# Optimization experiments

Measured on AMD Instinct MI355X. Metric: run time of the kernel, lower is better.

The kernel has to match this reference:

```python
import jax, jax.numpy as jnp
import numpy as np

BS, N, H, W, C3D, K = 2, 4096, 64, 192, 64, 3


def _leaky(x):
    return jnp.where(x >= 0, x, 0.1 * x)


def setup_inputs() -> dict:
    key = jax.random.key(0)
    ks = jax.random.split(key, 10)
    # uv: pixel coordinates (x in [0,W), y in [0,H)), channel-first [bs,2,N]
    uv = jax.random.uniform(ks[0], (BS, 2, N), dtype=jnp.float32)
    uv = uv * jnp.array([W, H], dtype=jnp.float32)[None, :, None]
    feat_2d = jax.random.normal(ks[1], (BS, 64, H, W), dtype=jnp.float32)
    feat_3d = jax.random.normal(ks[2], (BS, C3D, N), dtype=jnp.float32)
    w1 = jax.random.normal(ks[3], (16, 3), dtype=jnp.float32) * 0.3
    b1 = jax.random.normal(ks[4], (16,), dtype=jnp.float32) * 0.1
    w2 = jax.random.normal(ks[5], (C3D, 16), dtype=jnp.float32) * 0.2
    b2 = jax.random.normal(ks[6], (C3D,), dtype=jnp.float32) * 0.1
    w_out = jax.random.normal(ks[7], (C3D, C3D), dtype=jnp.float32) * 0.1
    b_out = jax.random.normal(ks[8], (C3D,), dtype=jnp.float32) * 0.1
    return {"uv": uv, "feat_2d": feat_2d, "feat_3d": feat_3d,
            "w1": w1, "b1": b1, "w2": w2, "b2": b2,
            "w_out": w_out, "b_out": b_out}


def reference(uv, feat_2d, feat_3d, w1, b1, w2, b2, w_out, b_out):
    bs, _, image_h, image_w = feat_2d.shape
    c3d = feat_3d.shape[1]
    hw = image_h * image_w

    # mesh grid, channel order (x, y), flattened row-major over (h, w): [bs,2,HW]
    ys, xs = jnp.meshgrid(jnp.arange(image_h, dtype=jnp.float32),
                          jnp.arange(image_w, dtype=jnp.float32), indexing='ij')
    grid = jnp.stack([xs.ravel(), ys.ravel()], axis=0)  # [2, HW]
    grid = jnp.broadcast_to(grid[None], (bs, 2, hw))

    # k-NN of uv points for each grid query: squared distances [bs, HW, N]
    d2 = (jnp.sum(grid * grid, axis=1)[:, :, None]
          + jnp.sum(uv * uv, axis=1)[:, None, :]
          - 2.0 * jnp.einsum('bcq,bcn->bqn', grid, uv))
    _, knn_idx = jax.lax.top_k(-d2, K)  # [bs, HW, K]

    # gather uv and feat_3d by neighbor indices: [bs, 2+C, HW, K]
    data = jnp.concatenate([uv, feat_3d], axis=1)
    knn = jax.vmap(lambda d, i: d[:, i])(data, knn_idx)
    knn_uv, knn_feat3d = knn[:, :2], knn[:, 2:]

    knn_offset = knn_uv - grid[..., None]                      # [bs,2,HW,K]
    offset_norm = jnp.linalg.norm(knn_offset, axis=1, keepdims=True)
    score_in = jnp.concatenate([knn_offset, offset_norm], 1)   # [bs,3,HW,K]

    # score net: 1x1 conv (3->16, leaky_relu 0.1) -> 1x1 conv (16->C, sigmoid)
    h1 = _leaky(jnp.einsum('bcqk,oc->boqk', score_in, w1) + b1[None, :, None, None])
    score = jax.nn.sigmoid(jnp.einsum('bcqk,oc->boqk', h1, w2) + b2[None, :, None, None])

    final = jnp.sum(score * knn_feat3d, axis=-1)               # [bs,C,HW]
    final = final.reshape(bs, c3d, image_h, image_w)

    # out conv: 1x1 conv (C->C) + leaky_relu 0.1
    out = _leaky(jnp.einsum('bchw,oc->bohw', final, w_out) + b_out[None, :, None, None])
    return out
```

## Files before the change

### kernel.cpp

```cpp
#include <hip/hip_runtime.h>
#include <math.h>

#define NBS 2
#define NPTS 4096
#define HH 64
#define WW 192
#define HW (HH*WW)
#define NC 64
#define GX 48
#define GY 16
#define NCELL (GX*GY)
#define CSB 1024

#define FBIG 3.0e38f
#define IBIG 0x7FFFFFFF

__global__ __launch_bounds__(256) void k0_prep(
    const float* __restrict__ uv, const float* __restrict__ f3d,
    float* __restrict__ f3dT, float4* __restrict__ binned,
    int* __restrict__ cellStart) {
#pragma clang fp contract(off)
  int bid = blockIdx.x;
  int t = threadIdx.x;
  if (bid < 2) {
    int b = bid;
    __shared__ int hist[NCELL];
    __shared__ int cum[NCELL];
    __shared__ int cur[NCELL];
    for (int c = t; c < NCELL; c += 256) hist[c] = 0;
    __syncthreads();
    const float* u0p = uv + (size_t)b * 2 * NPTS;
    const float* u1p = u0p + NPTS;
    for (int n = t; n < NPTS; n += 256) {
      float u0 = u0p[n], u1 = u1p[n];
      int cxp = min((int)(u0 * 0.25f), GX - 1);
      int cyp = min((int)(u1 * 0.25f), GY - 1);
      atomicAdd(&hist[cyp * GX + cxp], 1);
    }
    __syncthreads();
    if (t < 64) {
      int carry = 0;
#pragma unroll
      for (int ck = 0; ck < NCELL / 64; ++ck) {
        int v = hist[ck * 64 + t];
#pragma unroll
        for (int off = 1; off < 64; off <<= 1) {
          int u = __shfl_up(v, off);
          if (t >= off) v += u;
        }
        cum[ck * 64 + t] = v + carry;
        carry += __shfl(v, 63);
      }
    }
    __syncthreads();
    if (t == 0) cellStart[b * CSB] = 0;
    for (int c = t; c < NCELL; c += 256) {
      cellStart[b * CSB + c + 1] = cum[c];
      cur[c] = cum[c] - hist[c];
    }
    __syncthreads();
    for (int n = t; n < NPTS; n += 256) {
      float u0 = u0p[n], u1 = u1p[n];
      float s0 = u0 * u0;
      float s1 = u1 * u1;
      float uu = s0 + s1;
      int cxp = min((int)(u0 * 0.25f), GX - 1);
      int cyp = min((int)(u1 * 0.25f), GY - 1);
      int pos = atomicAdd(&cur[cyp * GX + cxp], 1);
      binned[(size_t)b * NPTS + pos] =
          make_float4(u0 + u0, u1 + u1, uu, __int_as_float(n));
    }
  } else {
    int bb = bid - 2;
    int b = bb >> 7;
    int half = (bb >> 6) & 1;
    int nt = (bb & 63) << 6;
    __shared__ float tile[32][65];
    int n_in = t & 63;
    int r0 = t >> 6;
    const float* src = f3d + (size_t)b * NC * NPTS + (size_t)half * 32 * NPTS;
#pragma unroll
    for (int r = 0; r < 8; ++r) {
      int c = r0 + (r << 2);
      tile[c][n_in] = src[(size_t)c * NPTS + nt + n_in];
    }
    __syncthreads();
    float* dst = f3dT + ((size_t)b * NPTS + nt) * NC + half * 32;
    int c_out = t & 31;
    int n0 = t >> 5;
#pragma unroll
    for (int r = 0; r < 8; ++r) {
      int n = n0 + (r << 3);
      dst[(size_t)n * NC + c_out] = tile[c_out][n];
    }
  }
}

__global__ __launch_bounds__(256) void k_main(
    const float4* __restrict__ binned, const int* __restrict__ cellStart,
    const float* __restrict__ uv, const float* __restrict__ f3dT,
    const float* __restrict__ w1, const float* __restrict__ b1,
    const float* __restrict__ w2, const float* __restrict__ b2,
    const float* __restrict__ w_out, const float* __restrict__ b_out,
    float* __restrict__ out) {
#pragma clang fp contract(off)
  int t = threadIdx.x;
  int b = blockIdx.y;
  int Q = t >> 4;
  int j = t & 15;
  int qi = blockIdx.x * 16 + Q;
  int x = qi % WW, y = qi / WW;
  float xf = (float)x, yf = (float)y;
  float gg = xf * xf + yf * yf;

  __shared__ float fin[16][68];

  float v0 = FBIG, v1 = FBIG, v2 = FBIG;
  int i0 = IBIG, i1 = IBIG, i2 = IBIG;
  {
    int cx = x >> 2, cy = y >> 2;
    const float4* __restrict__ pts = binned + (size_t)b * NPTS;
    const int* __restrict__ cs = cellStart + b * CSB;

    auto insS = [&](float d, int gi) {
      bool lt2 = (d < v2) || (d == v2 && gi < i2);
      bool lt1 = (d < v1) || (d == v1 && gi < i1);
      bool lt0 = (d < v0) || (d == v0 && gi < i0);
      i2 = lt1 ? i1 : (lt2 ? gi : i2);
      v2 = lt1 ? v1 : (lt2 ? d : v2);
      i1 = lt0 ? i0 : (lt1 ? gi : i1);
      v1 = lt0 ? v0 : (lt1 ? d : v1);
      i0 = lt0 ? gi : i0;
      v0 = lt0 ? d : v0;
    };
    auto insM = [&](float d, int gi) {
      bool dup = (gi == i0) || (gi == i1) || (gi == i2);
      bool lt2 = !dup && ((d < v2) || (d == v2 && gi < i2));
      bool lt1 = !dup && ((d < v1) || (d == v1 && gi < i1));
      bool lt0 = !dup && ((d < v0) || (d == v0 && gi < i0));
      i2 = lt1 ? i1 : (lt2 ? gi : i2);
      v2 = lt1 ? v1 : (lt2 ? d : v2);
      i1 = lt0 ? i0 : (lt1 ? gi : i1);
      v1 = lt0 ? v0 : (lt1 ? d : v1);
      i0 = lt0 ? gi : i0;
      v0 = lt0 ? d : v0;
    };
    auto scanRow = [&](int ry, int cA, int cB) {
      int s = cs[ry * GX + cA];
      int e = cs[ry * GX + cB + 1];
      for (int n = s + j; n < e; n += 16) {
        float4 p = pts[n];
        float d = (gg + p.z) - __builtin_fmaf(yf, p.y, xf * p.x);
        insS(d, __float_as_int(p.w));
      }
    };
    auto mergeAll = [&]() {
#pragma unroll
      for (int m = 1; m <= 8; m <<= 1) {
        float ov0 = __shfl_xor(v0, m), ov1 = __shfl_xor(v1, m),
              ov2 = __shfl_xor(v2, m);
        int oi0 = __shfl_xor(i0, m), oi1 = __shfl_xor(i1, m),
            oi2 = __shfl_xor(i2, m);
        insM(ov0, oi0); insM(ov1, oi1); insM(ov2, oi2);
      }
    };

    int cxL = max(cx - 1, 0), cxH = min(cx + 1, GX - 1);
    int cyL = max(cy - 1, 0), cyH = min(cy + 1, GY - 1);
    for (int ry = cyL; ry <= cyH; ++ry) scanRow(ry, cxL, cxH);
    mergeAll();

    while (true) {
      bool fullDom = (cxL == 0 && cxH == GX - 1 && cyL == 0 && cyH == GY - 1);
      float dL = (cxL > 0) ? (xf - (float)(cxL * 4)) : FBIG;
      float dR = (cxH < GX - 1) ? ((float)((cxH + 1) * 4) - xf) : FBIG;
      float dB = (cyL > 0) ? (yf - (float)(cyL * 4)) : FBIG;
      float dT = (cyH < GY - 1) ? ((float)((cyH + 1) * 4) - yf) : FBIG;
      float dmin = fminf(fminf(dL, dR), fminf(dB, dT));
      if (fullDom || (v2 < dmin * dmin - 1.0f)) break;
      int nxL = max(cxL - 1, 0), nxH = min(cxH + 1, GX - 1);
      int nyL = max(cyL - 1, 0), nyH = min(cyH + 1, GY - 1);
      for (int ry = nyL; ry <= nyH; ++ry) {
        if (ry < cyL || ry > cyH) scanRow(ry, nxL, nxH);
        else {
          if (nxL < cxL) scanRow(ry, nxL, cxL - 1);
          if (nxH > cxH) scanRow(ry, cxH + 1, nxH);
        }
      }
      cxL = nxL; cxH = nxH; cyL = nyL; cyH = nyH;
      mergeAll();
    }
  }

  {
    int idx[3] = {i0, i1, i2};
    float h1a[3][16];
#pragma unroll
    for (int k = 0; k < 3; ++k) {
      int i = idx[k];
      float u0 = uv[(size_t)b * 2 * NPTS + i];
      float u1 = uv[(size_t)b * 2 * NPTS + NPTS + i];
      float dx = u0 - xf;
      float dy = u1 - yf;
      float nrm = sqrtf(__builtin_fmaf(dx, dx, dy * dy));
#pragma unroll
      for (int o = 0; o < 16; ++o) {
        float h = fmaf(w1[o * 3 + 0], dx,
                 fmaf(w1[o * 3 + 1], dy,
                 fmaf(w1[o * 3 + 2], nrm, b1[o])));
        h1a[k][o] = (h >= 0.0f) ? h : 0.1f * h;
      }
    }

    float4 f0 = *(const float4*)(f3dT + ((size_t)b * NPTS + idx[0]) * NC + j * 4);
    float4 f1 = *(const float4*)(f3dT + ((size_t)b * NPTS + idx[1]) * NC + j * 4);
    float4 f2 = *(const float4*)(f3dT + ((size_t)b * NPTS + idx[2]) * NC + j * 4);
    float fa[4] = {f0.x, f0.y, f0.z, f0.w};
    float fb[4] = {f1.x, f1.y, f1.z, f1.w};
    float fc[4] = {f2.x, f2.y, f2.z, f2.w};
    float res[4];
#pragma unroll
    for (int cc = 0; cc < 4; ++cc) {
      int c = j * 4 + cc;
      float bias = b2[c];
      float s0 = bias, s1 = bias, s2 = bias;
      const float4* w2r = (const float4*)(w2 + c * 16);
#pragma unroll
      for (int o4 = 0; o4 < 4; ++o4) {
        float4 wv = w2r[o4];
        float wvs[4] = {wv.x, wv.y, wv.z, wv.w};
#pragma unroll
        for (int oo = 0; oo < 4; ++oo) {
          int o = o4 * 4 + oo;
          s0 = fmaf(wvs[oo], h1a[0][o], s0);
          s1 = fmaf(wvs[oo], h1a[1][o], s1);
          s2 = fmaf(wvs[oo], h1a[2][o], s2);
        }
      }
      float g0 = 1.0f / (1.0f + __expf(-s0));
      float g1 = 1.0f / (1.0f + __expf(-s1));
      float g2 = 1.0f / (1.0f + __expf(-s2));
      res[cc] = fmaf(g0, fa[cc], fmaf(g1, fb[cc], g2 * fc[cc]));
    }
    *(float4*)(&fin[Q][j * 4]) = make_float4(res[0], res[1], res[2], res[3]);
  }
  __syncthreads();

  {
    int qb = t & 15;
    int cgb = t >> 4;
    int q = blockIdx.x * 16 + qb;
    int o0 = cgb * 4;
    float acc[4];
#pragma unroll
    for (int jj = 0; jj < 4; ++jj) acc[jj] = b_out[o0 + jj];
    const float4* finq = (const float4*)(&fin[qb][0]);
#pragma unroll 4
    for (int c4 = 0; c4 < 16; ++c4) {
      float4 f = finq[c4];
#pragma unroll
      for (int jj = 0; jj < 4; ++jj) {
        float4 wv = *(const float4*)(w_out + (o0 + jj) * 64 + c4 * 4);
        acc[jj] = fmaf(wv.x, f.x,
                  fmaf(wv.y, f.y,
                  fmaf(wv.z, f.z,
                  fmaf(wv.w, f.w, acc[jj]))));
      }
    }
    float* dst = out + ((size_t)(b * 64 + o0)) * HW + q;
#pragma unroll
    for (int jj = 0; jj < 4; ++jj) {
      float v = acc[jj];
      dst[(size_t)jj * HW] = (v >= 0.0f) ? v : 0.1f * v;
    }
  }
}

extern "C" void kernel_launch(void* const* d_in, const int* in_sizes, int n_in,
                              void* d_out, int out_size, void* d_ws, size_t ws_size,
                              hipStream_t stream) {
  const float* uv   = (const float*)d_in[0];
  const float* f3d  = (const float*)d_in[2];
  const float* w1   = (const float*)d_in[3];
  const float* b1   = (const float*)d_in[4];
  const float* w2   = (const float*)d_in[5];
  const float* b2   = (const float*)d_in[6];
  const float* wout = (const float*)d_in[7];
  const float* bout = (const float*)d_in[8];
  float* out = (float*)d_out;

  char* ws = (char*)d_ws;
  float*  f3dT      = (float*)(ws);
  float4* binned    = (float4*)(ws + 2097152);
  int*    cellStart = (int*)(ws + 2228224);

  hipLaunchKernelGGL(k0_prep, dim3(258), dim3(256), 0, stream,
                     uv, f3d, f3dT, binned, cellStart);
  hipLaunchKernelGGL(k_main, dim3(HW / 16, NBS), dim3(256), 0, stream,
                     (const float4*)binned, (const int*)cellStart,
                     uv, f3dT, w1, b1, w2, b2, wout, bout, out);
}
```

Baseline: 52.45 us.

## Split fused kNN+MLP kernel into separate kNN and MLP kernels

Splits the main kernel into a kNN search kernel, where 4 lanes cooperate per query with 32 queries per 128-thread block, and an MLP kernel that reads neighbor indices from a workspace buffer. The first MLP layer is spread across lanes, one hidden unit per thread, and staged through shared memory, so each thread no longer computes all 16 hidden units redundantly. The aim is to cut shuffle-merge overhead and raise lane utilization in the irregular kNN scan. The cost is an extra kernel launch and an index round-trip through global memory, and with only 4 lanes per query the long candidate scans become more serial per thread.

```diff
diff --git a/kernel.cpp b/kernel.cpp
--- a/kernel.cpp
+++ b/kernel.cpp
@@ -96,105 +96,122 @@
   }
 }
 
-__global__ __launch_bounds__(256) void k_main(
+__global__ __launch_bounds__(128) void kA_knn(
     const float4* __restrict__ binned, const int* __restrict__ cellStart,
-    const float* __restrict__ uv, const float* __restrict__ f3dT,
+    int4* __restrict__ idxOut) {
+#pragma clang fp contract(off)
+  int t = threadIdx.x;
+  int Q = t >> 2;
+  int j = t & 3;
+  int qi = blockIdx.x * 32 + Q;
+  int b = blockIdx.y;
+  int x = qi % WW, y = qi / WW;
+  float xf = (float)x, yf = (float)y;
+  float gg = xf * xf + yf * yf;
+  int cx = x >> 2, cy = y >> 2;
+
+  const float4* __restrict__ pts = binned + (size_t)b * NPTS;
+  const int* __restrict__ cs = cellStart + b * CSB;
+
+  float v0 = FBIG, v1 = FBIG, v2 = FBIG;
+  int i0 = IBIG, i1 = IBIG, i2 = IBIG;
+
+  auto insS = [&](float d, int gi) {
+    bool lt2 = (d < v2) || (d == v2 && gi < i2);
+    bool lt1 = (d < v1) || (d == v1 && gi < i1);
+    bool lt0 = (d < v0) || (d == v0 && gi < i0);
+    i2 = lt1 ? i1 : (lt2 ? gi : i2);
+    v2 = lt1 ? v1 : (lt2 ? d : v2);
+    i1 = lt0 ? i0 : (lt1 ? gi : i1);
+    v1 = lt0 ? v0 : (lt1 ? d : v1);
+    i0 = lt0 ? gi : i0;
+    v0 = lt0 ? d : v0;
+  };
+  auto insM = [&](float d, int gi) {
+    bool dup = (gi == i0) || (gi == i1) || (gi == i2);
+    bool lt2 = !dup && ((d < v2) || (d == v2 && gi < i2));
+    bool lt1 = !dup && ((d < v1) || (d == v1 && gi < i1));
+    bool lt0 = !dup && ((d < v0) || (d == v0 && gi < i0));
+    i2 = lt1 ? i1 : (lt2 ? gi : i2);
+    v2 = lt1 ? v1 : (lt2 ? d : v2);
+    i1 = lt0 ? i0 : (lt1 ? gi : i1);
+    v1 = lt0 ? v0 : (lt1 ? d : v1);
+    i0 = lt0 ? gi : i0;
+    v0 = lt0 ? d : v0;
+  };
+  auto scanRow = [&](int ry, int cA, int cB) {
+    int s = cs[ry * GX + cA];
+    int e = cs[ry * GX + cB + 1];
+    for (int n = s + j; n < e; n += 4) {
+      float4 p = pts[n];
+      float d = (gg + p.z) - __builtin_fmaf(yf, p.y, xf * p.x);
+      insS(d, __float_as_int(p.w));
+    }
+  };
+  auto mergeAll = [&]() {
+#pragma unroll
+    for (int m = 1; m <= 2; m <<= 1) {
+      float ov0 = __shfl_xor(v0, m), ov1 = __shfl_xor(v1, m),
+            ov2 = __shfl_xor(v2, m);
+      int oi0 = __shfl_xor(i0, m), oi1 = __shfl_xor(i1, m),
+          oi2 = __shfl_xor(i2, m);
+      insM(ov0, oi0); insM(ov1, oi1); insM(ov2, oi2);
+    }
+  };
+
+  int cxL = max(cx - 1, 0), cxH = min(cx + 1, GX - 1);
+  int cyL = max(cy - 1, 0), cyH = min(cy + 1, GY - 1);
+  for (int ry = cyL; ry <= cyH; ++ry) scanRow(ry, cxL, cxH);
+  mergeAll();
+
+  while (true) {
+    bool fullDom = (cxL == 0 && cxH == GX - 1 && cyL == 0 && cyH == GY - 1);
+    float dL = (cxL > 0) ? (xf - (float)(cxL * 4)) : FBIG;
+    float dR = (cxH < GX - 1) ? ((float)((cxH + 1) * 4) - xf) : FBIG;
+    float dB = (cyL > 0) ? (yf - (float)(cyL * 4)) : FBIG;
+    float dT = (cyH < GY - 1) ? ((float)((cyH + 1) * 4) - yf) : FBIG;
+    float dmin = fminf(fminf(dL, dR), fminf(dB, dT));
+    if (fullDom || (v2 < dmin * dmin - 1.0f)) break;
+    int nxL = max(cxL - 1, 0), nxH = min(cxH + 1, GX - 1);
+    int nyL = max(cyL - 1, 0), nyH = min(cyH + 1, GY - 1);
+    for (int ry = nyL; ry <= nyH; ++ry) {
+      if (ry < cyL || ry > cyH) scanRow(ry, nxL, nxH);
+      else {
+        if (nxL < cxL) scanRow(ry, nxL, cxL - 1);
+        if (nxH > cxH) scanRow(ry, cxH + 1, nxH);
+      }
+    }
+    cxL = nxL; cxH = nxH; cyL = nyL; cyH = nyH;
+    mergeAll();
+  }
+
+  if (j == 0) idxOut[(size_t)b * HW + qi] = make_int4(i0, i1, i2, 0);
+}
+
+__global__ __launch_bounds__(256) void kB_mlp(
+    const int4* __restrict__ idx4, const float* __restrict__ uv,
+    const float* __restrict__ f3dT,
     const float* __restrict__ w1, const float* __restrict__ b1,
     const float* __restrict__ w2, const float* __restrict__ b2,
     const float* __restrict__ w_out, const float* __restrict__ b_out,
     float* __restrict__ out) {
-#pragma clang fp contract(off)
   int t = threadIdx.x;
   int b = blockIdx.y;
   int Q = t >> 4;
-  int j = t & 15;
+  int o = t & 15;
   int qi = blockIdx.x * 16 + Q;
-  int x = qi % WW, y = qi / WW;
-  float xf = (float)x, yf = (float)y;
-  float gg = xf * xf + yf * yf;
-
+  float xf = (float)(qi % WW);
+  float yf = (float)(qi / WW);
+
+  __shared__ float sh1f[16 * 52];
   __shared__ float fin[16][68];
 
-  float v0 = FBIG, v1 = FBIG, v2 = FBIG;
-  int i0 = IBIG, i1 = IBIG, i2 = IBIG;
+  int4 id4 = idx4[(size_t)b * HW + qi];
+  int idx[3] = {id4.x, id4.y, id4.z};
+
   {
-    int cx = x >> 2, cy = y >> 2;
-    const float4* __restrict__ pts = binned + (size_t)b * NPTS;
-    const int* __restrict__ cs = cellStart + b * CSB;
-
-    auto insS = [&](float d, int gi) {
-      bool lt2 = (d < v2) || (d == v2 && gi < i2);
-      bool lt1 = (d < v1) || (d == v1 && gi < i1);
-      bool lt0 = (d < v0) || (d == v0 && gi < i0);
-      i2 = lt1 ? i1 : (lt2 ? gi : i2);
-      v2 = lt1 ? v1 : (lt2 ? d : v2);
-      i1 = lt0 ? i0 : (lt1 ? gi : i1);
-      v1 = lt0 ? v0 : (lt1 ? d : v1);
-      i0 = lt0 ? gi : i0;
-      v0 = lt0 ? d : v0;
-    };
-    auto insM = [&](float d, int gi) {
-      bool dup = (gi == i0) || (gi == i1) || (gi == i2);
-      bool lt2 = !dup && ((d < v2) || (d == v2 && gi < i2));
-      bool lt1 = !dup && ((d < v1) || (d == v1 && gi < i1));
-      bool lt0 = !dup && ((d < v0) || (d == v0 && gi < i0));
-      i2 = lt1 ? i1 : (lt2 ? gi : i2);
-      v2 = lt1 ? v1 : (lt2 ? d : v2);
-      i1 = lt0 ? i0 : (lt1 ? gi : i1);
-      v1 = lt0 ? v0 : (lt1 ? d : v1);
-      i0 = lt0 ? gi : i0;
-      v0 = lt0 ? d : v0;
-    };
-    auto scanRow = [&](int ry, int cA, int cB) {
-      int s = cs[ry * GX + cA];
-      int e = cs[ry * GX + cB + 1];
-      for (int n = s + j; n < e; n += 16) {
-        float4 p = pts[n];
-        float d = (gg + p.z) - __builtin_fmaf(yf, p.y, xf * p.x);
-        insS(d, __float_as_int(p.w));
-      }
-    };
-    auto mergeAll = [&]() {
-#pragma unroll
-      for (int m = 1; m <= 8; m <<= 1) {
-        float ov0 = __shfl_xor(v0, m), ov1 = __shfl_xor(v1, m),
-              ov2 = __shfl_xor(v2, m);
-        int oi0 = __shfl_xor(i0, m), oi1 = __shfl_xor(i1, m),
-            oi2 = __shfl_xor(i2, m);
-        insM(ov0, oi0); insM(ov1, oi1); insM(ov2, oi2);
-      }
-    };
-
-    int cxL = max(cx - 1, 0), cxH = min(cx + 1, GX - 1);
-    int cyL = max(cy - 1, 0), cyH = min(cy + 1, GY - 1);
-    for (int ry = cyL; ry <= cyH; ++ry) scanRow(ry, cxL, cxH);
-    mergeAll();
-
-    while (true) {
-      bool fullDom = (cxL == 0 && cxH == GX - 1 && cyL == 0 && cyH == GY - 1);
-      float dL = (cxL > 0) ? (xf - (float)(cxL * 4)) : FBIG;
-      float dR = (cxH < GX - 1) ? ((float)((cxH + 1) * 4) - xf) : FBIG;
-      float dB = (cyL > 0) ? (yf - (float)(cyL * 4)) : FBIG;
-      float dT = (cyH < GY - 1) ? ((float)((cyH + 1) * 4) - yf) : FBIG;
-      float dmin = fminf(fminf(dL, dR), fminf(dB, dT));
-      if (fullDom || (v2 < dmin * dmin - 1.0f)) break;
-      int nxL = max(cxL - 1, 0), nxH = min(cxH + 1, GX - 1);
-      int nyL = max(cyL - 1, 0), nyH = min(cyH + 1, GY - 1);
-      for (int ry = nyL; ry <= nyH; ++ry) {
-        if (ry < cyL || ry > cyH) scanRow(ry, nxL, nxH);
-        else {
-          if (nxL < cxL) scanRow(ry, nxL, cxL - 1);
-          if (nxH > cxH) scanRow(ry, cxH + 1, nxH);
-        }
-      }
-      cxL = nxL; cxH = nxH; cyL = nyL; cyH = nyH;
-      mergeAll();
-    }
-  }
-
-  {
-    int idx[3] = {i0, i1, i2};
-    float h1a[3][16];
+    float wa = w1[o * 3 + 0], wb = w1[o * 3 + 1], wc = w1[o * 3 + 2];
+    float bo = b1[o];
 #pragma unroll
     for (int k = 0; k < 3; ++k) {
       int i = idx[k];
@@ -203,25 +220,34 @@
       float dx = u0 - xf;
       float dy = u1 - yf;
       float nrm = sqrtf(__builtin_fmaf(dx, dx, dy * dy));
-#pragma unroll
-      for (int o = 0; o < 16; ++o) {
-        float h = fmaf(w1[o * 3 + 0], dx,
-                 fmaf(w1[o * 3 + 1], dy,
-                 fmaf(w1[o * 3 + 2], nrm, b1[o])));
-        h1a[k][o] = (h >= 0.0f) ? h : 0.1f * h;
-      }
-    }
-
-    float4 f0 = *(const float4*)(f3dT + ((size_t)b * NPTS + idx[0]) * NC + j * 4);
-    float4 f1 = *(const float4*)(f3dT + ((size_t)b * NPTS + idx[1]) * NC + j * 4);
-    float4 f2 = *(const float4*)(f3dT + ((size_t)b * NPTS + idx[2]) * NC + j * 4);
+      float h = fmaf(wa, dx, fmaf(wb, dy, fmaf(wc, nrm, bo)));
+      sh1f[Q * 52 + k * 16 + o] = (h >= 0.0f) ? h : 0.1f * h;
+    }
+  }
+  __syncthreads();
+
+  {
+    float h1a[3][16];
+    {
+      const float4* h4 = (const float4*)(sh1f + Q * 52);
+#pragma unroll
+      for (int i = 0; i < 12; ++i) {
+        float4 v = h4[i];
+        int k = i >> 2, oo = (i & 3) * 4;
+        h1a[k][oo + 0] = v.x; h1a[k][oo + 1] = v.y;
+        h1a[k][oo + 2] = v.z; h1a[k][oo + 3] = v.w;
+      }
+    }
+    float4 f0 = *(const float4*)(f3dT + ((size_t)b * NPTS + idx[0]) * NC + o * 4);
+    float4 f1 = *(const float4*)(f3dT + ((size_t)b * NPTS + idx[1]) * NC + o * 4);
+    float4 f2 = *(const float4*)(f3dT + ((size_t)b * NPTS + idx[2]) * NC + o * 4);
     float fa[4] = {f0.x, f0.y, f0.z, f0.w};
     float fb[4] = {f1.x, f1.y, f1.z, f1.w};
     float fc[4] = {f2.x, f2.y, f2.z, f2.w};
     float res[4];
 #pragma unroll
     for (int cc = 0; cc < 4; ++cc) {
-      int c = j * 4 + cc;
+      int c = o * 4 + cc;
       float bias = b2[c];
       float s0 = bias, s1 = bias, s2 = bias;
       const float4* w2r = (const float4*)(w2 + c * 16);
@@ -231,10 +257,10 @@
         float wvs[4] = {wv.x, wv.y, wv.z, wv.w};
 #pragma unroll
         for (int oo = 0; oo < 4; ++oo) {
-          int o = o4 * 4 + oo;
-          s0 = fmaf(wvs[oo], h1a[0][o], s0);
-          s1 = fmaf(wvs[oo], h1a[1][o], s1);
-          s2 = fmaf(wvs[oo], h1a[2][o], s2);
+          int oi = o4 * 4 + oo;
+          s0 = fmaf(wvs[oo], h1a[0][oi], s0);
+          s1 = fmaf(wvs[oo], h1a[1][oi], s1);
+          s2 = fmaf(wvs[oo], h1a[2][oi], s2);
         }
       }
       float g0 = 1.0f / (1.0f + __expf(-s0));
@@ -242,7 +268,7 @@
       float g2 = 1.0f / (1.0f + __expf(-s2));
       res[cc] = fmaf(g0, fa[cc], fmaf(g1, fb[cc], g2 * fc[cc]));
     }
-    *(float4*)(&fin[Q][j * 4]) = make_float4(res[0], res[1], res[2], res[3]);
+    *(float4*)(&fin[Q][o * 4]) = make_float4(res[0], res[1], res[2], res[3]);
   }
   __syncthreads();
 
@@ -293,10 +319,12 @@
   float*  f3dT      = (float*)(ws);
   float4* binned    = (float4*)(ws + 2097152);
   int*    cellStart = (int*)(ws + 2228224);
+  int4*   idx4      = (int4*)(ws + 2236416);
 
   hipLaunchKernelGGL(k0_prep, dim3(258), dim3(256), 0, stream,
                      uv, f3d, f3dT, binned, cellStart);
-  hipLaunchKernelGGL(k_main, dim3(HW / 16, NBS), dim3(256), 0, stream,
-                     (const float4*)binned, (const int*)cellStart,
-                     uv, f3dT, w1, b1, w2, b2, wout, bout, out);
+  hipLaunchKernelGGL(kA_knn, dim3(HW / 32, NBS), dim3(128), 0, stream,
+                     (const float4*)binned, (const int*)cellStart, idx4);
+  hipLaunchKernelGGL(kB_mlp, dim3(HW / 16, NBS), dim3(256), 0, stream,
+                     (const int4*)idx4, uv, f3dT, w1, b1, w2, b2, wout, bout, out);
 }
```

New measurement: 54.17 us. 1.03x slower.

## Coarsen kNN grid cells to 8x8 and split first score layer across lanes

Applied to the files above, without the earlier changes.

Halves the spatial grid resolution used to bin uv points for kNN search (cells go from 4 to 8 pixels wide), so each query scans fewer, larger cells and needs fewer ring expansions. The prefix-sum over cells becomes a simple shared-memory Hillis-Steele scan over the smaller cell count. The first score-net layer is now computed once per (query, hidden unit) by each of the 16 lanes and shared through LDS, instead of every lane recomputing all 16 hidden units. This costs one extra barrier and more distance tests per scanned cell.

```diff
diff --git a/kernel.cpp b/kernel.cpp
--- a/kernel.cpp
+++ b/kernel.cpp
@@ -7,10 +7,10 @@
 #define WW 192
 #define HW (HH*WW)
 #define NC 64
-#define GX 48
-#define GY 16
+#define GX 24
+#define GY 8
 #define NCELL (GX*GY)
-#define CSB 1024
+#define CSB 256
 
 #define FBIG 3.0e38f
 #define IBIG 0x7FFFFFFF
@@ -24,48 +24,36 @@
   int t = threadIdx.x;
   if (bid < 2) {
     int b = bid;
-    __shared__ int hist[NCELL];
-    __shared__ int cum[NCELL];
+    __shared__ int hist[NCELL + 1];
     __shared__ int cur[NCELL];
-    for (int c = t; c < NCELL; c += 256) hist[c] = 0;
+    if (t <= NCELL) hist[t] = 0;
     __syncthreads();
     const float* u0p = uv + (size_t)b * 2 * NPTS;
     const float* u1p = u0p + NPTS;
     for (int n = t; n < NPTS; n += 256) {
       float u0 = u0p[n], u1 = u1p[n];
-      int cxp = min((int)(u0 * 0.25f), GX - 1);
-      int cyp = min((int)(u1 * 0.25f), GY - 1);
-      atomicAdd(&hist[cyp * GX + cxp], 1);
+      int cxp = min((int)(u0 * 0.125f), GX - 1);
+      int cyp = min((int)(u1 * 0.125f), GY - 1);
+      atomicAdd(&hist[cyp * GX + cxp + 1], 1);
     }
     __syncthreads();
-    if (t < 64) {
-      int carry = 0;
-#pragma unroll
-      for (int ck = 0; ck < NCELL / 64; ++ck) {
-        int v = hist[ck * 64 + t];
-#pragma unroll
-        for (int off = 1; off < 64; off <<= 1) {
-          int u = __shfl_up(v, off);
-          if (t >= off) v += u;
-        }
-        cum[ck * 64 + t] = v + carry;
-        carry += __shfl(v, 63);
-      }
-    }
-    __syncthreads();
-    if (t == 0) cellStart[b * CSB] = 0;
-    for (int c = t; c < NCELL; c += 256) {
-      cellStart[b * CSB + c + 1] = cum[c];
-      cur[c] = cum[c] - hist[c];
-    }
+    for (int off = 1; off <= NCELL; off <<= 1) {
+      int v = 0;
+      if (t <= NCELL && t >= off) v = hist[t - off];
+      __syncthreads();
+      if (t <= NCELL && t >= off) hist[t] += v;
+      __syncthreads();
+    }
+    if (t < NCELL) cur[t] = hist[t];
+    if (t <= NCELL) cellStart[b * CSB + t] = hist[t];
     __syncthreads();
     for (int n = t; n < NPTS; n += 256) {
       float u0 = u0p[n], u1 = u1p[n];
       float s0 = u0 * u0;
       float s1 = u1 * u1;
       float uu = s0 + s1;
-      int cxp = min((int)(u0 * 0.25f), GX - 1);
-      int cyp = min((int)(u1 * 0.25f), GY - 1);
+      int cxp = min((int)(u0 * 0.125f), GX - 1);
+      int cyp = min((int)(u1 * 0.125f), GY - 1);
       int pos = atomicAdd(&cur[cyp * GX + cxp], 1);
       binned[(size_t)b * NPTS + pos] =
           make_float4(u0 + u0, u1 + u1, uu, __int_as_float(n));
@@ -113,12 +101,13 @@
   float xf = (float)x, yf = (float)y;
   float gg = xf * xf + yf * yf;
 
+  __shared__ float sh1f[16 * 52];
   __shared__ float fin[16][68];
 
   float v0 = FBIG, v1 = FBIG, v2 = FBIG;
   int i0 = IBIG, i1 = IBIG, i2 = IBIG;
   {
-    int cx = x >> 2, cy = y >> 2;
+    int cx = x >> 3, cy = y >> 3;
     const float4* __restrict__ pts = binned + (size_t)b * NPTS;
     const int* __restrict__ cs = cellStart + b * CSB;
 
@@ -172,12 +161,12 @@
 
     while (true) {
       bool fullDom = (cxL == 0 && cxH == GX - 1 && cyL == 0 && cyH == GY - 1);
-      float dL = (cxL > 0) ? (xf - (float)(cxL * 4)) : FBIG;
-      float dR = (cxH < GX - 1) ? ((float)((cxH + 1) * 4) - xf) : FBIG;
-      float dB = (cyL > 0) ? (yf - (float)(cyL * 4)) : FBIG;
-      float dT = (cyH < GY - 1) ? ((float)((cyH + 1) * 4) - yf) : FBIG;
+      float dL = (cxL > 0) ? (xf - (float)(cxL * 8)) : FBIG;
+      float dR = (cxH < GX - 1) ? ((float)((cxH + 1) * 8) - xf) : FBIG;
+      float dB = (cyL > 0) ? (yf - (float)(cyL * 8)) : FBIG;
+      float dT = (cyH < GY - 1) ? ((float)((cyH + 1) * 8) - yf) : FBIG;
       float dmin = fminf(fminf(dL, dR), fminf(dB, dT));
-      if (fullDom || (v2 < dmin * dmin - 1.0f)) break;
+      if (fullDom || (v2 < dmin * dmin - 4.0f)) break;
       int nxL = max(cxL - 1, 0), nxH = min(cxH + 1, GX - 1);
       int nyL = max(cyL - 1, 0), nyH = min(cyH + 1, GY - 1);
       for (int ry = nyL; ry <= nyH; ++ry) {
@@ -193,8 +182,9 @@
   }
 
   {
+    float wa = w1[j * 3 + 0], wb = w1[j * 3 + 1], wc = w1[j * 3 + 2];
+    float bo = b1[j];
     int idx[3] = {i0, i1, i2};
-    float h1a[3][16];
 #pragma unroll
     for (int k = 0; k < 3; ++k) {
       int i = idx[k];
@@ -203,18 +193,27 @@
       float dx = u0 - xf;
       float dy = u1 - yf;
       float nrm = sqrtf(__builtin_fmaf(dx, dx, dy * dy));
-#pragma unroll
-      for (int o = 0; o < 16; ++o) {
-        float h = fmaf(w1[o * 3 + 0], dx,
-                 fmaf(w1[o * 3 + 1], dy,
-                 fmaf(w1[o * 3 + 2], nrm, b1[o])));
-        h1a[k][o] = (h >= 0.0f) ? h : 0.1f * h;
-      }
-    }
-
-    float4 f0 = *(const float4*)(f3dT + ((size_t)b * NPTS + idx[0]) * NC + j * 4);
-    float4 f1 = *(const float4*)(f3dT + ((size_t)b * NPTS + idx[1]) * NC + j * 4);
-    float4 f2 = *(const float4*)(f3dT + ((size_t)b * NPTS + idx[2]) * NC + j * 4);
+      float h = fmaf(wa, dx, fmaf(wb, dy, fmaf(wc, nrm, bo)));
+      sh1f[Q * 52 + k * 16 + j] = (h >= 0.0f) ? h : 0.1f * h;
+    }
+  }
+  __syncthreads();
+
+  {
+    float h1a[3][16];
+    {
+      const float4* h4 = (const float4*)(sh1f + Q * 52);
+#pragma unroll
+      for (int i = 0; i < 12; ++i) {
+        float4 v = h4[i];
+        int k = i >> 2, oo = (i & 3) * 4;
+        h1a[k][oo + 0] = v.x; h1a[k][oo + 1] = v.y;
+        h1a[k][oo + 2] = v.z; h1a[k][oo + 3] = v.w;
+      }
+    }
+    float4 f0 = *(const float4*)(f3dT + ((size_t)b * NPTS + i0) * NC + j * 4);
+    float4 f1 = *(const float4*)(f3dT + ((size_t)b * NPTS + i1) * NC + j * 4);
+    float4 f2 = *(const float4*)(f3dT + ((size_t)b * NPTS + i2) * NC + j * 4);
     float fa[4] = {f0.x, f0.y, f0.z, f0.w};
     float fb[4] = {f1.x, f1.y, f1.z, f1.w};
     float fc[4] = {f2.x, f2.y, f2.z, f2.w};
@@ -231,10 +230,10 @@
         float wvs[4] = {wv.x, wv.y, wv.z, wv.w};
 #pragma unroll
         for (int oo = 0; oo < 4; ++oo) {
-          int o = o4 * 4 + oo;
-          s0 = fmaf(wvs[oo], h1a[0][o], s0);
-          s1 = fmaf(wvs[oo], h1a[1][o], s1);
-          s2 = fmaf(wvs[oo], h1a[2][o], s2);
+          int oi = o4 * 4 + oo;
+          s0 = fmaf(wvs[oo], h1a[0][oi], s0);
+          s1 = fmaf(wvs[oo], h1a[1][oi], s1);
+          s2 = fmaf(wvs[oo], h1a[2][oi], s2);
         }
       }
       float g0 = 1.0f / (1.0f + __expf(-s0));
```

Measured after the change: 56.58 us. +7.9%, slower.
